# Kernel tuning notes

Hardware: AMD Instinct MI355X
Metric: run time of the kernel (lower is better)

## Reference

```python
import jax, jax.numpy as jnp
import numpy as np

OBS_LEN = 20
PRED_LEN = 30
NUM_MODES = 6
DATA_DIM = 2
DROPOUT_P = 0.25
NEG_SLOPE = 0.01
H_DIM = 256
B = 8192


def setup_inputs() -> dict:
    key = jax.random.key(0)
    ks = jax.random.split(key, 20)
    s = 0.05
    inp = {
        "traj_abs": jax.random.normal(ks[0], (OBS_LEN, B, DATA_DIM), jnp.float32),
        "traj_rel": jax.random.normal(ks[1], (OBS_LEN, B, DATA_DIM), jnp.float32),
        "state_h": jax.random.normal(ks[2], (1, B, H_DIM), jnp.float32),
        "c0": jax.random.normal(ks[3], (NUM_MODES, B, H_DIM), jnp.float32),
        # spatial embedding Linear(40, 40)
        "W_se": jax.random.normal(ks[4], (OBS_LEN * 2, OBS_LEN * 2), jnp.float32) * s,
        "b_se": jax.random.normal(ks[5], (OBS_LEN * 2,), jnp.float32) * s,
        # LSTM weights: input 40 -> hidden 256, gates order i,f,g,o
        "W_ih": jax.random.normal(ks[6], (4 * H_DIM, OBS_LEN * 2), jnp.float32) * s,
        "W_hh": jax.random.normal(ks[7], (4 * H_DIM, H_DIM), jnp.float32) * s,
        "b_ih": jax.random.normal(ks[8], (4 * H_DIM,), jnp.float32) * s,
        "b_hh": jax.random.normal(ks[9], (4 * H_DIM,), jnp.float32) * s,
        # per-mode prediction heads Linear(256, 2)
        "W_pred": jax.random.normal(ks[10], (NUM_MODES, DATA_DIM, H_DIM), jnp.float32) * s,
        "b_pred": jax.random.normal(ks[11], (NUM_MODES, DATA_DIM), jnp.float32) * s,
        # confidence PredictionNet (norm=False), latent = PRED_LEN*DATA_DIM = 60
        "pn_w1": jax.random.normal(ks[12], (PRED_LEN * DATA_DIM, PRED_LEN * DATA_DIM), jnp.float32) * s,
        "pn_b1": jax.random.normal(ks[13], (PRED_LEN * DATA_DIM,), jnp.float32) * s,
        "pn_w2": jax.random.normal(ks[14], (PRED_LEN * DATA_DIM, PRED_LEN * DATA_DIM), jnp.float32) * s,
        "pn_b2": jax.random.normal(ks[15], (PRED_LEN * DATA_DIM,), jnp.float32) * s,
        "pn_wfc": jax.random.normal(ks[16], (1, PRED_LEN * DATA_DIM), jnp.float32) * s,
        "pn_bfc": jax.random.normal(ks[17], (1,), jnp.float32) * s,
    }
    return inp


def _decode(traj_rel, state_h, c0, W_se, b_se, W_ih, W_hh, b_ih, b_hh,
            W_pred, b_pred, pn_w1, pn_b1, pn_w2, pn_b2, pn_wfc, pn_bfc):
    batch = traj_rel.shape[1]
    h0 = state_h[0]  # (B, H)
    keep = 1.0 - DROPOUT_P
    # one dropout key per (mode, step); deterministic stand-in for torch dropout
    keys = jax.random.split(jax.random.key(42), NUM_MODES * PRED_LEN).reshape(NUM_MODES, PRED_LEN)

    def one_mode(Wp, bp, c0m, keys_m):
        def step(carry, key):
            h, c, buf = carry  # buf: (OBS_LEN, B, 2) rolling window of rel displacements
            x = buf.transpose(1, 0, 2).reshape(batch, -1) @ W_se.T + b_se  # (B, 40)
            x = jnp.where(x > 0, x, NEG_SLOPE * x)  # leaky_relu
            mask = jax.random.bernoulli(key, keep, x.shape)
            x = jnp.where(mask, x / keep, 0.0)  # dropout (training=True)
            gates = x @ W_ih.T + b_ih + h @ W_hh.T + b_hh  # (B, 4H)
            i, f, g, o = jnp.split(gates, 4, axis=-1)
            c = jax.nn.sigmoid(f) * c + jax.nn.sigmoid(i) * jnp.tanh(g)
            h = jax.nn.sigmoid(o) * jnp.tanh(c)
            rel = h @ Wp.T + bp  # (B, 2)
            buf = jnp.roll(buf, -1, axis=0).at[-1].set(rel)
            return (h, c, buf), rel

        _, rels = jax.lax.scan(step, (h0, c0m, traj_rel), keys_m)
        return rels  # (PRED_LEN, B, 2)

    rels = jax.vmap(one_mode)(W_pred, b_pred, c0, keys)  # (M, T, B, 2)
    pred = rels.transpose(2, 0, 1, 3)  # (B, M, T, 2)

    # confidence PredictionNet (norm=False)
    x = pred.reshape(batch, NUM_MODES, PRED_LEN * DATA_DIM)
    y = jax.nn.relu(x @ pn_w1.T + pn_b1)
    y = jax.nn.relu(y @ pn_w2.T + pn_b2 + x)
    conf = (y @ pn_wfc.T + pn_bfc).reshape(batch, NUM_MODES)
    conf = jax.nn.softmax(conf, axis=1)
    return pred, conf


def reference(traj_abs, traj_rel, state_h, c0, W_se, b_se, W_ih, W_hh, b_ih, b_hh,
              W_pred, b_pred, pn_w1, pn_b1, pn_w2, pn_b2, pn_wfc, pn_bfc):
    # traj_abs unused in the 'Latent' branch (only its shape is read)
    return _decode(traj_rel, state_h, c0, W_se, b_se, W_ih, W_hh, b_ih, b_hh,
                   W_pred, b_pred, pn_w1, pn_b1, pn_w2, pn_b2, pn_wfc, pn_bfc)
```

## Files before the change

kernel.cpp:

```cpp
#include <hip/hip_runtime.h>
#include <cstdint>

#define JAX_PARTITIONABLE 1

#define OBS_LEN 20
#define PRED_LEN 30
#define NUM_MODES 6
#define BATCH 8192
#define H 256
#define MB (NUM_MODES * BATCH)
#define KPAD 320

typedef __attribute__((ext_vector_type(8))) short bf16x8;
typedef __attribute__((ext_vector_type(4))) float f32x4;

__host__ __device__ inline void tf2x32(uint32_t k0, uint32_t k1, uint32_t c0, uint32_t c1,
                                       uint32_t& o0, uint32_t& o1) {
  uint32_t ks0 = k0, ks1 = k1, ks2 = k0 ^ k1 ^ 0x1BD11BDAu;
  uint32_t x0 = c0 + ks0, x1 = c1 + ks1;
#define TF_R(x, r) (((x) << (r)) | ((x) >> (32 - (r))))
#define TF_RND(r)  { x0 += x1; x1 = TF_R(x1, r); x1 ^= x0; }
  TF_RND(13) TF_RND(15) TF_RND(26) TF_RND(6)   x0 += ks1; x1 += ks2 + 1u;
  TF_RND(17) TF_RND(29) TF_RND(16) TF_RND(24)  x0 += ks2; x1 += ks0 + 2u;
  TF_RND(13) TF_RND(15) TF_RND(26) TF_RND(6)   x0 += ks0; x1 += ks1 + 3u;
  TF_RND(17) TF_RND(29) TF_RND(16) TF_RND(24)  x0 += ks1; x1 += ks2 + 4u;
  TF_RND(13) TF_RND(15) TF_RND(26) TF_RND(6)   x0 += ks2; x1 += ks0 + 5u;
  o0 = x0; o1 = x1;
#undef TF_RND
#undef TF_R
}

__device__ inline void step_key(int m, int t, uint32_t& k0, uint32_t& k1) {
#if JAX_PARTITIONABLE
  tf2x32(0u, 42u, 0u, (uint32_t)(m * PRED_LEN + t), k0, k1);
#else
  int i = m * PRED_LEN + t;
  int n0 = 2 * i, n1 = 2 * i + 1;
  uint32_t a0, a1;
  if (n0 < 180) { tf2x32(0u, 42u, (uint32_t)n0, (uint32_t)(n0 + 180), a0, a1); k0 = a0; }
  else          { tf2x32(0u, 42u, (uint32_t)(n0 - 180), (uint32_t)n0, a0, a1); k0 = a1; }
  if (n1 < 180) { tf2x32(0u, 42u, (uint32_t)n1, (uint32_t)(n1 + 180), a0, a1); k1 = a0; }
  else          { tf2x32(0u, 42u, (uint32_t)(n1 - 180), (uint32_t)n1, a0, a1); k1 = a1; }
#endif
}

__device__ inline uint32_t mask_bits(uint32_t k0, uint32_t k1, uint32_t n) {
#if JAX_PARTITIONABLE
  uint32_t o0, o1;
  tf2x32(k0, k1, 0u, n, o0, o1);
  return o0 ^ o1;
#else
  const uint32_t HALF = (uint32_t)(BATCH * 40 / 2);
  uint32_t o0, o1;
  if (n < HALF) { tf2x32(k0, k1, n, n + HALF, o0, o1); return o0; }
  else          { tf2x32(k0, k1, n - HALF, n, o0, o1); return o1; }
#endif
}

__device__ __forceinline__ float sigf(float x) { return 1.0f / (1.0f + __expf(-x)); }
__device__ __forceinline__ float tanhfast(float x) {
  float e = __expf(-2.0f * fabsf(x));
  float t = (1.0f - e) / (1.0f + e);
  return x >= 0.f ? t : -t;
}
__device__ __forceinline__ ushort f2bf(float f) {
  uint32_t u = __float_as_uint(f);
  uint32_t r = (u + 0x7fffu + ((u >> 16) & 1u)) >> 16;
  return (ushort)r;
}
__device__ __forceinline__ float bf2f(uint32_t u) { return __uint_as_float(u << 16); }

__global__ __launch_bounds__(256) void k_prep(const float* __restrict__ Wih, const float* __restrict__ Whh,
                                              const float* __restrict__ bih, const float* __restrict__ bhh,
                                              ushort* __restrict__ WTb, float* __restrict__ bias) {
  int idx = blockIdx.x * 256 + threadIdx.x;
  if (idx < 1024 * KPAD) {
    int np = idx / KPAD, k = idx - np * KPAD;
    int cg = np >> 7, r = np & 127;
    int nt = r >> 4, col = r & 15;
    int N = (nt & 3) * 256 + cg * 32 + (nt >> 2) * 16 + col;
    float v = (k < 40) ? Wih[N * 40 + k] : (k < 296 ? Whh[N * 256 + (k - 40)] : 0.f);
    WTb[idx] = f2bf(v);
  }
  if (idx < 1024) bias[idx] = bih[idx] + bhh[idx];
}

__global__ __launch_bounds__(256) void k_init(const float* __restrict__ state_h, const float* __restrict__ c0,
                                              float* __restrict__ cst, ushort* __restrict__ Ab0,
                                              ushort* __restrict__ Ab1) {
  int idx = blockIdx.x * 256 + threadIdx.x;
  if (idx < MB * 64) {
    int row = idx >> 6;
    int j4 = (idx & 63) << 2;
    float4 cv = *(const float4*)(c0 + (size_t)idx * 4);
    *(float4*)(cst + (size_t)idx * 4) = cv;
    int b = row & (BATCH - 1);
    float4 hv = *(const float4*)(state_h + (size_t)b * H + j4);
    ushort4 hb = {f2bf(hv.x), f2bf(hv.y), f2bf(hv.z), f2bf(hv.w)};
    *(ushort4*)(Ab0 + (size_t)row * KPAD + 40 + j4) = hb;
  }
  if (idx < MB * 6) {
    int row = idx / 6, p4 = (idx - row * 6) << 2;
    ushort4 z = {0, 0, 0, 0};
    *(ushort4*)(Ab0 + (size_t)row * KPAD + 296 + p4) = z;
    *(ushort4*)(Ab1 + (size_t)row * KPAD + 296 + p4) = z;
  }
}

__global__ __launch_bounds__(256) void k_embed(const float* __restrict__ traj_rel, const float* __restrict__ rels,
                                               const float* __restrict__ Wse, const float* __restrict__ bse,
                                               ushort* __restrict__ Ax, int t) {
  __shared__ float sW[1600];
  __shared__ float sb[40];
  int tid = threadIdx.x;
  for (int i = tid; i < 1600; i += 256) sW[i] = Wse[i];
  if (tid < 40) sb[tid] = bse[tid];
  __syncthreads();
  int gid = blockIdx.x * 256 + tid;
  int b = gid & (BATCH - 1);
  int m = gid >> 13;
  float win[40];
#pragma unroll
  for (int kk = 0; kk < OBS_LEN; kk++) {
    int st = t + kk;
    const float* p = (st < OBS_LEN)
        ? (traj_rel + (((size_t)st * BATCH + b) << 1))
        : (rels + (((size_t)(m * PRED_LEN + (st - OBS_LEN)) * BATCH + b) << 1));
    float2 w = *(const float2*)p;
    win[kk * 2] = w.x; win[kk * 2 + 1] = w.y;
  }
  uint32_t k0, k1;
  step_key(m, t, k0, k1);
  uint32_t nb = (uint32_t)(b * 40);
  ushort* orow = Ax + (size_t)gid * KPAD;
#pragma unroll
  for (int jo = 0; jo < 5; jo++) {
    uint32_t pk[4];
#pragma unroll
    for (int jp = 0; jp < 4; jp++) {
      ushort lo = 0, hi = 0;
#pragma unroll
      for (int ji = 0; ji < 2; ji++) {
        int j = jo * 8 + jp * 2 + ji;
        float a = sb[j];
#pragma unroll
        for (int p = 0; p < 40; p += 4) {
          float4 w = *(const float4*)&sW[j * 40 + p];
          a = fmaf(win[p + 3], w.w, fmaf(win[p + 2], w.z, fmaf(win[p + 1], w.y, fmaf(win[p], w.x, a))));
        }
        a = a > 0.f ? a : 0.01f * a;
        uint32_t bits = mask_bits(k0, k1, nb + (uint32_t)j);
        float u = __uint_as_float((bits >> 9) | 0x3f800000u) - 1.0f;
        ushort r = (u < 0.75f) ? f2bf(a * 1.3333333730697632f) : (ushort)0;
        if (ji == 0) lo = r; else hi = r;
      }
      pk[jp] = (uint32_t)lo | ((uint32_t)hi << 16);
    }
    uint4 v = {pk[0], pk[1], pk[2], pk[3]};
    *(uint4*)(orow + jo * 8) = v;
  }
}

__global__ __launch_bounds__(256) void k_gates(const ushort* __restrict__ Ain, const ushort* __restrict__ WTb,
                                               const float* __restrict__ bias, float* __restrict__ cst,
                                               ushort* __restrict__ Anext) {
  __shared__ __align__(16) ushort lA[2][128][40];
  __shared__ __align__(16) ushort lB[2][128][40];
  int tid = threadIdx.x;
  int w = tid >> 6, lane = tid & 63;
  int row0 = blockIdx.x * 128;
  int cg = blockIdx.y;
  int sr = tid >> 1, sh = (tid & 1) << 4;
  const ushort* gA = Ain + (size_t)(row0 + sr) * KPAD + sh;
  const ushort* gB = WTb + (size_t)(cg * 128 + sr) * KPAD + sh;

  f32x4 zero = {0.f, 0.f, 0.f, 0.f};
  f32x4 acc[2][8];
#pragma unroll
  for (int i = 0; i < 2; i++)
#pragma unroll
    for (int j = 0; j < 8; j++) acc[i][j] = zero;

  uint4 ra0 = *(const uint4*)gA;
  uint4 ra1 = *(const uint4*)(gA + 8);
  uint4 rb0 = *(const uint4*)gB;
  uint4 rb1 = *(const uint4*)(gB + 8);
  *(uint4*)&lA[0][sr][sh] = ra0;
  *(uint4*)&lA[0][sr][sh + 8] = ra1;
  *(uint4*)&lB[0][sr][sh] = rb0;
  *(uint4*)&lB[0][sr][sh + 8] = rb1;
  __syncthreads();

  int fm = lane & 15, fq = lane >> 4;
  for (int kt = 0; kt < 10; kt++) {
    int cur = kt & 1;
    if (kt < 9) {
      ra0 = *(const uint4*)(gA + (kt + 1) * 32);
      ra1 = *(const uint4*)(gA + (kt + 1) * 32 + 8);
      rb0 = *(const uint4*)(gB + (kt + 1) * 32);
      rb1 = *(const uint4*)(gB + (kt + 1) * 32 + 8);
    }
    bf16x8 af[2], bfr[8];
#pragma unroll
    for (int rt = 0; rt < 2; rt++) af[rt] = *(const bf16x8*)&lA[cur][w * 32 + rt * 16 + fm][fq * 8];
#pragma unroll
    for (int nt = 0; nt < 8; nt++) bfr[nt] = *(const bf16x8*)&lB[cur][nt * 16 + fm][fq * 8];
#pragma unroll
    for (int rt = 0; rt < 2; rt++)
#pragma unroll
      for (int nt = 0; nt < 8; nt++)
        acc[rt][nt] = __builtin_amdgcn_mfma_f32_16x16x32_bf16(af[rt], bfr[nt], acc[rt][nt], 0, 0, 0);
    if (kt < 9) {
      *(uint4*)&lA[cur ^ 1][sr][sh] = ra0;
      *(uint4*)&lA[cur ^ 1][sr][sh + 8] = ra1;
      *(uint4*)&lB[cur ^ 1][sr][sh] = rb0;
      *(uint4*)&lB[cur ^ 1][sr][sh + 8] = rb1;
      __syncthreads();
    }
  }

#pragma unroll
  for (int jg = 0; jg < 2; jg++) {
    int jh = cg * 32 + jg * 16 + fm;
    float bi = bias[jh], bfg = bias[256 + jh], bg = bias[512 + jh], bo = bias[768 + jh];
#pragma unroll
    for (int rt = 0; rt < 2; rt++) {
#pragma unroll
      for (int reg = 0; reg < 4; reg++) {
        int row = row0 + w * 32 + rt * 16 + fq * 4 + reg;
        float gi = acc[rt][jg * 4 + 0][reg] + bi;
        float gf = acc[rt][jg * 4 + 1][reg] + bfg;
        float gg = acc[rt][jg * 4 + 2][reg] + bg;
        float go = acc[rt][jg * 4 + 3][reg] + bo;
        size_t ci = (size_t)row * H + jh;
        float cv = cst[ci];
        float c2 = sigf(gf) * cv + sigf(gi) * tanhfast(gg);
        cst[ci] = c2;
        float hn = sigf(go) * tanhfast(c2);
        Anext[(size_t)row * KPAD + 40 + jh] = f2bf(hn);
      }
    }
  }
}

__global__ __launch_bounds__(256) void k_pred(const ushort* __restrict__ hsrc, const float* __restrict__ Wp,
                                              const float* __restrict__ bp, float* __restrict__ rels, int t) {
  int tid = threadIdx.x;
  int wv = tid >> 6, lane = tid & 63;
  int grp = lane >> 3, lg = lane & 7;
  int row = blockIdx.x * 32 + wv * 8 + grp;
  int m = row / BATCH, b = row & (BATCH - 1);
  const ushort* hr = hsrc + (size_t)row * KPAD + 40 + lg * 32;
  const float* w0 = Wp + m * 512 + lg * 32;
  const float* w1 = w0 + 256;
  float s0 = 0.f, s1 = 0.f;
#pragma unroll
  for (int q = 0; q < 4; q++) {
    uint4 hv = *(const uint4*)(hr + q * 8);
    float h0 = bf2f(hv.x & 0xffffu), h1 = bf2f(hv.x >> 16);
    float h2 = bf2f(hv.y & 0xffffu), h3 = bf2f(hv.y >> 16);
    float h4 = bf2f(hv.z & 0xffffu), h5 = bf2f(hv.z >> 16);
    float h6 = bf2f(hv.w & 0xffffu), h7 = bf2f(hv.w >> 16);
    float4 wa0 = *(const float4*)(w0 + q * 8);
    float4 wa1 = *(const float4*)(w0 + q * 8 + 4);
    float4 wb0 = *(const float4*)(w1 + q * 8);
    float4 wb1 = *(const float4*)(w1 + q * 8 + 4);
    s0 += h0 * wa0.x + h1 * wa0.y + h2 * wa0.z + h3 * wa0.w
        + h4 * wa1.x + h5 * wa1.y + h6 * wa1.z + h7 * wa1.w;
    s1 += h0 * wb0.x + h1 * wb0.y + h2 * wb0.z + h3 * wb0.w
        + h4 * wb1.x + h5 * wb1.y + h6 * wb1.z + h7 * wb1.w;
  }
#pragma unroll
  for (int off = 1; off < 8; off <<= 1) {
    s0 += __shfl_xor(s0, off, 64);
    s1 += __shfl_xor(s1, off, 64);
  }
  if (lg == 0) {
    float2 r = make_float2(s0 + bp[m * 2], s1 + bp[m * 2 + 1]);
    *(float2*)(rels + ((size_t)(m * PRED_LEN + t) * BATCH + b) * 2) = r;
  }
}

__global__ __launch_bounds__(256) void k_transconf(const float* __restrict__ rels,
                                                   const float* __restrict__ W1, const float* __restrict__ b1,
                                                   const float* __restrict__ W2, const float* __restrict__ b2,
                                                   const float* __restrict__ wfc, const float* __restrict__ bfc,
                                                   float* __restrict__ out) {
  __shared__ float tile[32][361];
  __shared__ float sW1[3600];
  __shared__ float sW2[3600];
  __shared__ float sb1[60], sb2[60], swfc[60];
  __shared__ float sy1[192][61];
  __shared__ float slg[32][6];
  int tid = threadIdx.x;
  for (int i = tid; i < 3600; i += 256) { sW1[i] = W1[i]; sW2[i] = W2[i]; }
  if (tid < 60) { sb1[tid] = b1[tid]; sb2[tid] = b2[tid]; swfc[tid] = wfc[tid]; }
  int b0 = blockIdx.x * 32;
  for (int i = tid; i < 11520; i += 256) {
    int bl = i & 31, c = i >> 5;
    int mm = c / 60, r = c % 60;
    tile[bl][c] = rels[((size_t)((mm * PRED_LEN + (r >> 1)) * BATCH) + (b0 + bl)) * 2 + (r & 1)];
  }
  __syncthreads();
  for (int i = tid; i < 11520; i += 256) {
    int bl = i / 360, c = i % 360;
    out[(size_t)(b0 + bl) * 360 + c] = tile[bl][c];
  }
  if (tid < 192) {
    int bl = tid / 6, mm = tid - bl * 6;
    int xb = mm * 60;
    for (int q = 0; q < 60; q++) {
      float acl = sb1[q];
#pragma unroll
      for (int p = 0; p < 60; p++) acl = fmaf(tile[bl][xb + p], sW1[q * 60 + p], acl);
      sy1[tid][q] = fmaxf(acl, 0.f);
    }
    float logit = bfc[0];
    for (int q = 0; q < 60; q++) {
      float acl = sb2[q] + tile[bl][xb + q];
#pragma unroll
      for (int p = 0; p < 60; p++) acl = fmaf(sy1[tid][p], sW2[q * 60 + p], acl);
      logit = fmaf(fmaxf(acl, 0.f), swfc[q], logit);
    }
    slg[bl][mm] = logit;
  }
  __syncthreads();
  if (tid < 32) {
    float mx = slg[tid][0];
#pragma unroll
    for (int m = 1; m < 6; m++) mx = fmaxf(mx, slg[tid][m]);
    float e[6], s = 0.f;
#pragma unroll
    for (int m = 0; m < 6; m++) { e[m] = __expf(slg[tid][m] - mx); s += e[m]; }
    float inv = 1.0f / s;
    size_t base = (size_t)BATCH * 360 + (size_t)(b0 + tid) * 6;
#pragma unroll
    for (int m = 0; m < 6; m++) out[base + m] = e[m] * inv;
  }
}

extern "C" void kernel_launch(void* const* d_in, const int* in_sizes, int n_in,
                              void* d_out, int out_size, void* d_ws, size_t ws_size,
                              hipStream_t stream) {
  const float* traj_rel = (const float*)d_in[1];
  const float* state_h  = (const float*)d_in[2];
  const float* c0       = (const float*)d_in[3];
  const float* Wse      = (const float*)d_in[4];
  const float* bse      = (const float*)d_in[5];
  const float* Wih      = (const float*)d_in[6];
  const float* Whh      = (const float*)d_in[7];
  const float* bih      = (const float*)d_in[8];
  const float* bhh      = (const float*)d_in[9];
  const float* Wp       = (const float*)d_in[10];
  const float* bp       = (const float*)d_in[11];
  const float* W1       = (const float*)d_in[12];
  const float* b1       = (const float*)d_in[13];
  const float* W2       = (const float*)d_in[14];
  const float* b2       = (const float*)d_in[15];
  const float* wfc      = (const float*)d_in[16];
  const float* bfc      = (const float*)d_in[17];
  float* out = (float*)d_out;

  float* cst  = (float*)d_ws;
  float* rels = cst + (size_t)MB * H;
  float* bias = rels + (size_t)NUM_MODES * PRED_LEN * BATCH * 2;
  ushort* WTb = (ushort*)(bias + 1024);
  ushort* Ab0 = WTb + (size_t)1024 * KPAD;
  ushort* Ab1 = Ab0 + (size_t)MB * KPAD;

  k_prep<<<1280, 256, 0, stream>>>(Wih, Whh, bih, bhh, WTb, bias);
  k_init<<<12288, 256, 0, stream>>>(state_h, c0, cst, Ab0, Ab1);
  for (int t = 0; t < PRED_LEN; t++) {
    ushort* Acur  = (t & 1) ? Ab1 : Ab0;
    ushort* Anext = (t & 1) ? Ab0 : Ab1;
    k_embed<<<192, 256, 0, stream>>>(traj_rel, rels, Wse, bse, Acur, t);
    k_gates<<<dim3(384, 8), 256, 0, stream>>>(Acur, WTb, bias, cst, Anext);
    k_pred<<<1536, 256, 0, stream>>>(Anext, Wp, bp, rels, t);
  }
  k_transconf<<<256, 256, 0, stream>>>(rels, W1, b1, W2, b2, wfc, bfc, out);
}
```

Before: 3.536 ms.

## Keep full A row tile in LDS and stream pre-swizzled weight fragments from global

The gate GEMM now loads a 64-row by 320-wide A tile into shared memory once per block and loops over all 256 hidden columns inside the block. Weight fragments are pre-arranged in k_prep into MFMA lane order, so each wave reads its B operand straight from global or L2 with register double buffering. The A operand is no longer re-read by 8 column-group blocks, which cuts global traffic and the per-k-step barriers. In exchange, every block streams the entire weight matrix through L2 and relies on cache hits for B, and the grid drops to 768 blocks.

```diff
diff --git a/kernel.cpp b/kernel.cpp
--- a/kernel.cpp
+++ b/kernel.cpp
@@ -75,10 +75,15 @@
                                               ushort* __restrict__ WTb, float* __restrict__ bias) {
   int idx = blockIdx.x * 256 + threadIdx.x;
   if (idx < 1024 * KPAD) {
-    int np = idx / KPAD, k = idx - np * KPAD;
-    int cg = np >> 7, r = np & 127;
-    int nt = r >> 4, col = r & 15;
-    int N = (nt & 3) * 256 + cg * 32 + (nt >> 2) * 16 + col;
+    int e = idx & 7;
+    int lane = (idx >> 3) & 63;
+    int t1 = idx >> 9;
+    int kt = t1 % 10;
+    int t2 = t1 / 10;
+    int g = t2 & 3, jt = t2 >> 2;
+    int fm = lane & 15, fq = lane >> 4;
+    int k = kt * 32 + fq * 8 + e;
+    int N = g * 256 + jt * 16 + fm;
     float v = (k < 40) ? Wih[N * 40 + k] : (k < 296 ? Whh[N * 256 + (k - 40)] : 0.f);
     WTb[idx] = f2bf(v);
   }
@@ -164,74 +169,68 @@
 __global__ __launch_bounds__(256) void k_gates(const ushort* __restrict__ Ain, const ushort* __restrict__ WTb,
                                                const float* __restrict__ bias, float* __restrict__ cst,
                                                ushort* __restrict__ Anext) {
-  __shared__ __align__(16) ushort lA[2][128][40];
-  __shared__ __align__(16) ushort lB[2][128][40];
+  __shared__ __align__(16) ushort lA[64][328];
   int tid = threadIdx.x;
   int w = tid >> 6, lane = tid & 63;
-  int row0 = blockIdx.x * 128;
-  int cg = blockIdx.y;
-  int sr = tid >> 1, sh = (tid & 1) << 4;
-  const ushort* gA = Ain + (size_t)(row0 + sr) * KPAD + sh;
-  const ushort* gB = WTb + (size_t)(cg * 128 + sr) * KPAD + sh;
-
-  f32x4 zero = {0.f, 0.f, 0.f, 0.f};
-  f32x4 acc[2][8];
-#pragma unroll
-  for (int i = 0; i < 2; i++)
-#pragma unroll
-    for (int j = 0; j < 8; j++) acc[i][j] = zero;
-
-  uint4 ra0 = *(const uint4*)gA;
-  uint4 ra1 = *(const uint4*)(gA + 8);
-  uint4 rb0 = *(const uint4*)gB;
-  uint4 rb1 = *(const uint4*)(gB + 8);
-  *(uint4*)&lA[0][sr][sh] = ra0;
-  *(uint4*)&lA[0][sr][sh + 8] = ra1;
-  *(uint4*)&lB[0][sr][sh] = rb0;
-  *(uint4*)&lB[0][sr][sh + 8] = rb1;
+  int fm = lane & 15, fq = lane >> 4;
+  int r0 = blockIdx.x * 64;
+
+  const ushort* gA0 = Ain + (size_t)r0 * KPAD;
+#pragma unroll
+  for (int i = 0; i < 10; i++) {
+    int o = (tid + i * 256) * 8;
+    int row = o / 320, col = o - row * 320;
+    *(uint4*)&lA[row][col] = *(const uint4*)(gA0 + o);
+  }
   __syncthreads();
 
-  int fm = lane & 15, fq = lane >> 4;
-  for (int kt = 0; kt < 10; kt++) {
-    int cur = kt & 1;
-    if (kt < 9) {
-      ra0 = *(const uint4*)(gA + (kt + 1) * 32);
-      ra1 = *(const uint4*)(gA + (kt + 1) * 32 + 8);
-      rb0 = *(const uint4*)(gB + (kt + 1) * 32);
-      rb1 = *(const uint4*)(gB + (kt + 1) * 32 + 8);
-    }
-    bf16x8 af[2], bfr[8];
-#pragma unroll
-    for (int rt = 0; rt < 2; rt++) af[rt] = *(const bf16x8*)&lA[cur][w * 32 + rt * 16 + fm][fq * 8];
-#pragma unroll
-    for (int nt = 0; nt < 8; nt++) bfr[nt] = *(const bf16x8*)&lB[cur][nt * 16 + fm][fq * 8];
-#pragma unroll
-    for (int rt = 0; rt < 2; rt++)
-#pragma unroll
-      for (int nt = 0; nt < 8; nt++)
-        acc[rt][nt] = __builtin_amdgcn_mfma_f32_16x16x32_bf16(af[rt], bfr[nt], acc[rt][nt], 0, 0, 0);
-    if (kt < 9) {
-      *(uint4*)&lA[cur ^ 1][sr][sh] = ra0;
-      *(uint4*)&lA[cur ^ 1][sr][sh + 8] = ra1;
-      *(uint4*)&lB[cur ^ 1][sr][sh] = rb0;
-      *(uint4*)&lB[cur ^ 1][sr][sh + 8] = rb1;
-      __syncthreads();
-    }
-  }
-
-#pragma unroll
-  for (int jg = 0; jg < 2; jg++) {
-    int jh = cg * 32 + jg * 16 + fm;
-    float bi = bias[jh], bfg = bias[256 + jh], bg = bias[512 + jh], bo = bias[768 + jh];
-#pragma unroll
-    for (int rt = 0; rt < 2; rt++) {
+#define LOADB(dst, kt) { \
+    dst[0] = *(const bf16x8*)(bb + (0 * 10 + (kt)) * 512); \
+    dst[1] = *(const bf16x8*)(bb + (1 * 10 + (kt)) * 512); \
+    dst[2] = *(const bf16x8*)(bb + (2 * 10 + (kt)) * 512); \
+    dst[3] = *(const bf16x8*)(bb + (3 * 10 + (kt)) * 512); }
+#define STEPK(src, kt) { \
+    bf16x8 af[4]; \
+    _Pragma("unroll") for (int rt = 0; rt < 4; rt++) \
+      af[rt] = *(const bf16x8*)&lA[rt * 16 + fm][(kt) * 32 + fq * 8]; \
+    _Pragma("unroll") for (int rt = 0; rt < 4; rt++) \
+      _Pragma("unroll") for (int g = 0; g < 4; g++) \
+        acc[rt][g] = __builtin_amdgcn_mfma_f32_16x16x32_bf16(af[rt], src[g], acc[rt][g], 0, 0, 0); }
+
+  for (int cb = 0; cb < 4; cb++) {
+    int jh0 = cb * 64 + w * 16;
+    const ushort* bb = WTb + (size_t)(cb * 4 + w) * 40 * 512 + lane * 8;
+    f32x4 zero = {0.f, 0.f, 0.f, 0.f};
+    f32x4 acc[4][4];
+#pragma unroll
+    for (int rt = 0; rt < 4; rt++)
+#pragma unroll
+      for (int g = 0; g < 4; g++) acc[rt][g] = zero;
+
+    bf16x8 bA[4], bB[4];
+    LOADB(bA, 0); LOADB(bB, 1);
+    STEPK(bA, 0); LOADB(bA, 2);
+    STEPK(bB, 1); LOADB(bB, 3);
+    STEPK(bA, 2); LOADB(bA, 4);
+    STEPK(bB, 3); LOADB(bB, 5);
+    STEPK(bA, 4); LOADB(bA, 6);
+    STEPK(bB, 5); LOADB(bB, 7);
+    STEPK(bA, 6); LOADB(bA, 8);
+    STEPK(bB, 7); LOADB(bB, 9);
+    STEPK(bA, 8);
+    STEPK(bB, 9);
+
+    int jh = jh0 + fm;
+    float bi = bias[jh], bff = bias[256 + jh], bg = bias[512 + jh], bo = bias[768 + jh];
+#pragma unroll
+    for (int rt = 0; rt < 4; rt++) {
 #pragma unroll
       for (int reg = 0; reg < 4; reg++) {
-        int row = row0 + w * 32 + rt * 16 + fq * 4 + reg;
-        float gi = acc[rt][jg * 4 + 0][reg] + bi;
-        float gf = acc[rt][jg * 4 + 1][reg] + bfg;
-        float gg = acc[rt][jg * 4 + 2][reg] + bg;
-        float go = acc[rt][jg * 4 + 3][reg] + bo;
+        int row = r0 + rt * 16 + fq * 4 + reg;
+        float gi = acc[rt][0][reg] + bi;
+        float gf = acc[rt][1][reg] + bff;
+        float gg = acc[rt][2][reg] + bg;
+        float go = acc[rt][3][reg] + bo;
         size_t ci = (size_t)row * H + jh;
         float cv = cst[ci];
         float c2 = sigf(gf) * cv + sigf(gi) * tanhfast(gg);
@@ -241,6 +240,8 @@
       }
     }
   }
+#undef LOADB
+#undef STEPK
 }
 
 __global__ __launch_bounds__(256) void k_pred(const ushort* __restrict__ hsrc, const float* __restrict__ Wp,
@@ -374,7 +375,7 @@
     ushort* Acur  = (t & 1) ? Ab1 : Ab0;
     ushort* Anext = (t & 1) ? Ab0 : Ab1;
     k_embed<<<192, 256, 0, stream>>>(traj_rel, rels, Wse, bse, Acur, t);
-    k_gates<<<dim3(384, 8), 256, 0, stream>>>(Acur, WTb, bias, cst, Anext);
+    k_gates<<<768, 256, 0, stream>>>(Acur, WTb, bias, cst, Anext);
     k_pred<<<1536, 256, 0, stream>>>(Anext, Wp, bp, rels, t);
   }
   k_transconf<<<256, 256, 0, stream>>>(rels, W1, b1, W2, b2, wfc, bfc, out);
```

Result: slower. 4.528 ms (+28.1%).

## Fuse embed into pred kernel, pair gate columns, swap gates grid order

Applied to the files above, without the earlier changes.

Merges the spatial-embedding and dropout step for the next timestep into the prediction-head kernel, so each step launches two kernels instead of three and the fresh rel is reused directly from registers. Weight rows are permuted so each lane owns adjacent hidden pairs, which lets the cell state, bias and h writes use float2/uint32 vector accesses. The gates grid is transposed so the column-group blocks sharing one A row tile are launched together, improving L2 reuse of activations. The fused kernel also writes the first 40 columns of the next A buffer that the gates kernel of the next step reads, so it depends on correct step ordering.

```diff
diff --git a/kernel.cpp b/kernel.cpp
--- a/kernel.cpp
+++ b/kernel.cpp
@@ -78,7 +78,7 @@
     int np = idx / KPAD, k = idx - np * KPAD;
     int cg = np >> 7, r = np & 127;
     int nt = r >> 4, col = r & 15;
-    int N = (nt & 3) * 256 + cg * 32 + (nt >> 2) * 16 + col;
+    int N = (nt & 3) * 256 + cg * 32 + col * 2 + (nt >> 2);
     float v = (k < 40) ? Wih[N * 40 + k] : (k < 296 ? Whh[N * 256 + (k - 40)] : 0.f);
     WTb[idx] = f2bf(v);
   }
@@ -168,8 +168,8 @@
   __shared__ __align__(16) ushort lB[2][128][40];
   int tid = threadIdx.x;
   int w = tid >> 6, lane = tid & 63;
-  int row0 = blockIdx.x * 128;
-  int cg = blockIdx.y;
+  int cg = blockIdx.x;
+  int row0 = blockIdx.y * 128;
   int sr = tid >> 1, sh = (tid & 1) << 4;
   const ushort* gA = Ain + (size_t)(row0 + sr) * KPAD + sh;
   const ushort* gB = WTb + (size_t)(cg * 128 + sr) * KPAD + sh;
@@ -219,37 +219,52 @@
     }
   }
 
-#pragma unroll
-  for (int jg = 0; jg < 2; jg++) {
-    int jh = cg * 32 + jg * 16 + fm;
-    float bi = bias[jh], bfg = bias[256 + jh], bg = bias[512 + jh], bo = bias[768 + jh];
-#pragma unroll
-    for (int rt = 0; rt < 2; rt++) {
-#pragma unroll
-      for (int reg = 0; reg < 4; reg++) {
-        int row = row0 + w * 32 + rt * 16 + fq * 4 + reg;
-        float gi = acc[rt][jg * 4 + 0][reg] + bi;
-        float gf = acc[rt][jg * 4 + 1][reg] + bfg;
-        float gg = acc[rt][jg * 4 + 2][reg] + bg;
-        float go = acc[rt][jg * 4 + 3][reg] + bo;
-        size_t ci = (size_t)row * H + jh;
-        float cv = cst[ci];
-        float c2 = sigf(gf) * cv + sigf(gi) * tanhfast(gg);
-        cst[ci] = c2;
-        float hn = sigf(go) * tanhfast(c2);
-        Anext[(size_t)row * KPAD + 40 + jh] = f2bf(hn);
-      }
-    }
-  }
-}
-
-__global__ __launch_bounds__(256) void k_pred(const ushort* __restrict__ hsrc, const float* __restrict__ Wp,
-                                              const float* __restrict__ bp, float* __restrict__ rels, int t) {
+  int p = cg * 16 + fm;
+  const float2* bias2 = (const float2*)bias;
+  float2 bi = bias2[p], bff = bias2[128 + p], bgg = bias2[256 + p], boo = bias2[384 + p];
+  float2* cst2 = (float2*)cst;
+#pragma unroll
+  for (int rt = 0; rt < 2; rt++) {
+#pragma unroll
+    for (int reg = 0; reg < 4; reg++) {
+      int row = row0 + w * 32 + rt * 16 + fq * 4 + reg;
+      float2 cv = cst2[(size_t)row * 128 + p];
+      float gi0 = acc[rt][0][reg] + bi.x;
+      float gf0 = acc[rt][1][reg] + bff.x;
+      float gg0 = acc[rt][2][reg] + bgg.x;
+      float go0 = acc[rt][3][reg] + boo.x;
+      float gi1 = acc[rt][4][reg] + bi.y;
+      float gf1 = acc[rt][5][reg] + bff.y;
+      float gg1 = acc[rt][6][reg] + bgg.y;
+      float go1 = acc[rt][7][reg] + boo.y;
+      float c20 = sigf(gf0) * cv.x + sigf(gi0) * tanhfast(gg0);
+      float c21 = sigf(gf1) * cv.y + sigf(gi1) * tanhfast(gg1);
+      float2 cw = make_float2(c20, c21);
+      cst2[(size_t)row * 128 + p] = cw;
+      float hn0 = sigf(go0) * tanhfast(c20);
+      float hn1 = sigf(go1) * tanhfast(c21);
+      uint32_t hp = (uint32_t)f2bf(hn0) | ((uint32_t)f2bf(hn1) << 16);
+      *(uint32_t*)(Anext + (size_t)row * KPAD + 40 + 2 * p) = hp;
+    }
+  }
+}
+
+__global__ __launch_bounds__(256) void k_predembed(const ushort* __restrict__ hsrc, const float* __restrict__ Wp,
+                                                   const float* __restrict__ bp, float* __restrict__ rels,
+                                                   const float* __restrict__ traj_rel,
+                                                   const float* __restrict__ Wse, const float* __restrict__ bse,
+                                                   ushort* __restrict__ Ax, int t) {
+  __shared__ float sW[1600];
+  __shared__ float sb[40];
   int tid = threadIdx.x;
+  for (int i = tid; i < 1600; i += 256) sW[i] = Wse[i];
+  if (tid < 40) sb[tid] = bse[tid];
+  __syncthreads();
   int wv = tid >> 6, lane = tid & 63;
   int grp = lane >> 3, lg = lane & 7;
   int row = blockIdx.x * 32 + wv * 8 + grp;
   int m = row / BATCH, b = row & (BATCH - 1);
+
   const ushort* hr = hsrc + (size_t)row * KPAD + 40 + lg * 32;
   const float* w0 = Wp + m * 512 + lg * 32;
   const float* w1 = w0 + 256;
@@ -275,9 +290,44 @@
     s0 += __shfl_xor(s0, off, 64);
     s1 += __shfl_xor(s1, off, 64);
   }
+  float relx = s0 + bp[m * 2];
+  float rely = s1 + bp[m * 2 + 1];
   if (lg == 0) {
-    float2 r = make_float2(s0 + bp[m * 2], s1 + bp[m * 2 + 1]);
-    *(float2*)(rels + ((size_t)(m * PRED_LEN + t) * BATCH + b) * 2) = r;
+    *(float2*)(rels + ((size_t)(m * PRED_LEN + t) * BATCH + b) * 2) = make_float2(relx, rely);
+  }
+
+  int te = t + 1;
+  float win[40];
+#pragma unroll
+  for (int kk = 0; kk < OBS_LEN; kk++) {
+    int st = te + kk;
+    float2 w2;
+    if (st < OBS_LEN) {
+      w2 = *(const float2*)(traj_rel + (((size_t)st * BATCH + b) << 1));
+    } else if (st - OBS_LEN == t) {
+      w2 = make_float2(relx, rely);
+    } else {
+      w2 = *(const float2*)(rels + (((size_t)(m * PRED_LEN + (st - OBS_LEN)) * BATCH + b) << 1));
+    }
+    win[kk * 2] = w2.x; win[kk * 2 + 1] = w2.y;
+  }
+  uint32_t k0, k1;
+  step_key(m, te, k0, k1);
+  uint32_t nb = (uint32_t)(b * 40);
+  ushort* orow = Ax + (size_t)row * KPAD;
+#pragma unroll
+  for (int u = 0; u < 5; u++) {
+    int j = lg * 5 + u;
+    float a = sb[j];
+#pragma unroll
+    for (int p = 0; p < 40; p += 4) {
+      float4 w = *(const float4*)&sW[j * 40 + p];
+      a = fmaf(win[p + 3], w.w, fmaf(win[p + 2], w.z, fmaf(win[p + 1], w.y, fmaf(win[p], w.x, a))));
+    }
+    a = a > 0.f ? a : 0.01f * a;
+    uint32_t bits = mask_bits(k0, k1, nb + (uint32_t)j);
+    float uu = __uint_as_float((bits >> 9) | 0x3f800000u) - 1.0f;
+    orow[j] = (uu < 0.75f) ? f2bf(a * 1.3333333730697632f) : (ushort)0;
   }
 }
 
@@ -370,12 +420,12 @@
 
   k_prep<<<1280, 256, 0, stream>>>(Wih, Whh, bih, bhh, WTb, bias);
   k_init<<<12288, 256, 0, stream>>>(state_h, c0, cst, Ab0, Ab1);
+  k_embed<<<192, 256, 0, stream>>>(traj_rel, rels, Wse, bse, Ab0, 0);
   for (int t = 0; t < PRED_LEN; t++) {
     ushort* Acur  = (t & 1) ? Ab1 : Ab0;
     ushort* Anext = (t & 1) ? Ab0 : Ab1;
-    k_embed<<<192, 256, 0, stream>>>(traj_rel, rels, Wse, bse, Acur, t);
-    k_gates<<<dim3(384, 8), 256, 0, stream>>>(Acur, WTb, bias, cst, Anext);
-    k_pred<<<1536, 256, 0, stream>>>(Anext, Wp, bp, rels, t);
+    k_gates<<<dim3(8, 384), 256, 0, stream>>>(Acur, WTb, bias, cst, Anext);
+    k_predembed<<<1536, 256, 0, stream>>>(Anext, Wp, bp, rels, traj_rel, Wse, bse, Anext, t);
   }
   k_transconf<<<256, 256, 0, stream>>>(rels, W1, b1, W2, b2, wfc, bfc, out);
 }
```

Result: no change. 3.526 ms (-0.3%).
